# Performance work log

Hardware: AMD Instinct MI355X
Metric: run time of the kernel (lower is better)

## Reference

```python
import jax, jax.numpy as jnp
import numpy as np

B, T, DC, DS, H, V = 8, 1024, 128, 128, 512, 50000
LENGTHS = np.array([2, 4])  # dictionary word lengths for slot 0 and slot 1
LMAX = 4                    # ring-buffer size >= max word length


def setup_inputs() -> dict:
    key = jax.random.key(0)
    ks = jax.random.split(key, 12)
    s = 0.05
    return {
        "char_emb": jax.random.normal(ks[0], (B, T, DC), jnp.float32),
        "word_ids": jax.random.randint(ks[1], (B, T, 2), 0, V),
        "sense_table": jax.random.normal(ks[2], (V, DS), jnp.float32),
        "w_ih": jax.random.normal(ks[3], (DC, 3 * H), jnp.float32) * s,
        "w_hh": jax.random.normal(ks[4], (H, 3 * H), jnp.float32) * s,
        "b": jnp.zeros((3 * H,), jnp.float32),
        "aw_ih": jax.random.normal(ks[5], (DC, H), jnp.float32) * s,
        "aw_hh": jax.random.normal(ks[6], (H, H), jnp.float32) * s,
        "ab": jnp.zeros((H,), jnp.float32),
        "ww_ih": jax.random.normal(ks[7], (DS, 3 * H), jnp.float32) * s,
        "ww_hh": jax.random.normal(ks[8], (H, 3 * H), jnp.float32) * s,
        "wb": jnp.zeros((3 * H,), jnp.float32),
    }


def _forward(char_emb, word_ids, sense_table, w_ih, w_hh, b,
             aw_ih, aw_hh, ab, ww_ih, ww_hh, wb):
    H_ = w_hh.shape[0]
    T_ = char_emb.shape[1]
    lengths = jnp.asarray(LENGTHS)
    slot_idx = jnp.arange(2)

    def run_seq(x_seq, wid_seq):
        # pend: ring buffer of pending word-cell states [LMAX, 2, H]
        def step(carry, t):
            h, c, pend, pmask = carry
            x = x_seq[t]
            # --- MultiInputLSTMCell (char cell) ---
            gates = x @ w_ih + h @ w_hh + b              # [3H]
            i = jax.nn.sigmoid(gates[:H_])
            o = jax.nn.sigmoid(gates[H_:2 * H_])
            g = jnp.tanh(gates[2 * H_:])
            r = jnp.mod(t, LMAX)
            cins = pend[r]                                # [2, H] incoming word cells
            m = pmask[r].astype(x.dtype)                  # [2] validity
            alpha = jax.nn.sigmoid(x @ aw_ih + ab + cins @ aw_hh)  # [2, H]
            ea = jnp.exp(alpha) * m[:, None]
            ei = jnp.exp(i)
            denom = ei + ea.sum(0)
            c_lat = (ei * g + (ea * cins).sum(0)) / denom
            c_plain = (1.0 - i) * c + i * g               # c_num == 0 path: f = 1 - i
            c1 = jnp.where(pmask[r].any(), c_lat, c_plain)
            h1 = o * jnp.tanh(c1)
            # consume the ring slot for this timestep
            pend = pend.at[r].set(0.0)
            pmask = pmask.at[r].set(False)
            # --- WordLSTMCell for words starting at t ---
            xw = sense_table[wid_seq[t]]                  # [2, DS]
            wg = xw @ ww_ih + h1 @ ww_hh + wb             # [2, 3H]
            f = jax.nn.sigmoid(wg[:, :H_])
            iw = jax.nn.sigmoid(wg[:, H_:2 * H_])
            gw = jnp.tanh(wg[:, 2 * H_:])
            cw = f * c1 + iw * gw                         # [2, H]
            ends = t + lengths - 1
            valid = ends < T_
            wslots = jnp.mod(ends, LMAX)
            old = pend[wslots, slot_idx]
            pend = pend.at[wslots, slot_idx].set(jnp.where(valid[:, None], cw, old))
            pmask = pmask.at[wslots, slot_idx].set(valid | pmask[wslots, slot_idx])
            return (h1, c1, pend, pmask), (h1, c1)

        carry0 = (jnp.zeros((H_,), x_seq.dtype), jnp.zeros((H_,), x_seq.dtype),
                  jnp.zeros((LMAX, 2, H_), x_seq.dtype), jnp.zeros((LMAX, 2), bool))
        _, (hs, cs) = jax.lax.scan(step, carry0, jnp.arange(T_))
        return hs, cs

    hs, cs = jax.vmap(run_seq)(char_emb, word_ids)
    return jnp.stack((hs, cs))  # [2, B, T, H]


def reference(char_emb, word_ids, sense_table, w_ih, w_hh, b,
              aw_ih, aw_hh, ab, ww_ih, ww_hh, wb):
    return _forward(char_emb, word_ids, sense_table, w_ih, w_hh, b,
                    aw_ih, aw_hh, ab, ww_ih, ww_hh, wb)
```

## Files before the change

kernel.cpp:

```cpp
#include <hip/hip_runtime.h>
#include <hip/hip_bf16.h>


#define Bq 8
#define Tq 1024
#define DCq 128
#define Hq 512
#define NWG 32
#define NTHR 256

typedef unsigned long long u64;

#define HPUB_OFF  0u
#define PENDP_OFF 65536u
#define WIHT_OFF  327680u
#define WHHT_OFF  720896u
#define AWIHT_OFF 2293760u
#define AWHHT_OFF 2424832u
#define WWIHT_OFF 2949120u
#define WWHHT_OFF 3342336u

__device__ __forceinline__ float bflo(unsigned u){ return __uint_as_float(u << 16); }
__device__ __forceinline__ float bfhi(unsigned u){ return __uint_as_float(u & 0xffff0000u); }
__device__ __forceinline__ float sigm(float x){ return 1.0f / (1.0f + __expf(-x)); }

__device__ __forceinline__ unsigned f2bf(float f){
  unsigned u = __float_as_uint(f);
  u += 0x7fffu + ((u >> 16) & 1u);
  return u >> 16;
}

__device__ __forceinline__ void fma4(float& acc, uint2 w, float4 v){
  acc = fmaf(bflo(w.x), v.x, acc);
  acc = fmaf(bfhi(w.x), v.y, acc);
  acc = fmaf(bflo(w.y), v.z, acc);
  acc = fmaf(bfhi(w.y), v.w, acc);
}

__device__ __forceinline__ float red16(float x){
  x += __shfl_xor(x, 8, 16);
  x += __shfl_xor(x, 4, 16);
  x += __shfl_xor(x, 2, 16);
  x += __shfl_xor(x, 1, 16);
  return x;
}

__device__ __forceinline__ u64 pack64(float v, unsigned gen){
  return ((u64)gen << 32) | (u64)__float_as_uint(v);
}
__device__ __forceinline__ void st64(u64* p, u64 w){
  __hip_atomic_store(p, w, __ATOMIC_RELAXED, __HIP_MEMORY_SCOPE_AGENT);
}
__device__ __forceinline__ void pub64(u64* p, float v, unsigned gen){
  st64(p, pack64(v, gen));
}
__device__ __forceinline__ u64 ld64(const u64* p){
  return __hip_atomic_load(p, __ATOMIC_RELAXED, __HIP_MEMORY_SCOPE_AGENT);
}
__device__ __forceinline__ unsigned genof(u64 v){ return (unsigned)(v >> 32); }
__device__ __forceinline__ float valof(u64 v){ return __uint_as_float((unsigned)v); }

__global__ void transpose_bf16(const float* __restrict__ src, __hip_bfloat16* __restrict__ dst,
                               int kshift, int total, int N){
  const int K = 1 << kshift;
  for (int idx = blockIdx.x * blockDim.x + threadIdx.x; idx < total;
       idx += gridDim.x * blockDim.x){
    int n = idx >> kshift;
    int k = idx & (K - 1);
    dst[idx] = __float2bfloat16(src[(size_t)k * N + n]);
  }
}

__global__ void __launch_bounds__(NTHR, 1)
lattice_main(const float* __restrict__ char_emb,
             const int*   __restrict__ word_ids,
             const float* __restrict__ sense_table,
             const float* __restrict__ bias_b,
             const float* __restrict__ bias_ab,
             const float* __restrict__ bias_wb,
             unsigned char* __restrict__ ws,
             float* __restrict__ out)
{
  const int seq  = blockIdx.x;
  const int wg   = blockIdx.y;
  const int tid  = threadIdx.x;
  const int grp  = tid >> 4;
  const int lane = tid & 15;
  const int J    = wg * 16 + grp;
  const int i0   = tid * 2, i1 = tid * 2 + 1;

  u64* hpub = (u64*)(ws + HPUB_OFF)  + (size_t)seq * 2 * 256;
  u64* pnd  = (u64*)(ws + PENDP_OFF) + (size_t)seq * 4 * 2 * Hq;

  const uint2* w_ihT  = (const uint2*)(ws + WIHT_OFF);
  const uint2* w_hhT  = (const uint2*)(ws + WHHT_OFF);
  const uint2* aw_ihT = (const uint2*)(ws + AWIHT_OFF);
  const uint2* aw_hhT = (const uint2*)(ws + AWHHT_OFF);
  const uint2* ww_ihT = (const uint2*)(ws + WWIHT_OFF);
  const uint2* ww_hhT = (const uint2*)(ws + WWHHT_OFF);

  uint2 Rwhh_i[8], Rwhh_o[8], Rwhh_g[8], Rawhh[8];
  uint2 Rwwh_f[8], Rwwh_i[8], Rwwh_g[8];
  uint2 Rwih_i[2], Rwih_o[2], Rwih_g[2], Rawih[2];
  uint2 Rwwi_f[2], Rwwi_i[2], Rwwi_g[2];
  {
    const uint2* whh_i = w_hhT  + (size_t)(0*Hq + J) * 128;
    const uint2* whh_o = w_hhT  + (size_t)(1*Hq + J) * 128;
    const uint2* whh_g = w_hhT  + (size_t)(2*Hq + J) * 128;
    const uint2* awhh  = aw_hhT + (size_t)J * 128;
    const uint2* wwh_f = ww_hhT + (size_t)(0*Hq + J) * 128;
    const uint2* wwh_i = ww_hhT + (size_t)(1*Hq + J) * 128;
    const uint2* wwh_g = ww_hhT + (size_t)(2*Hq + J) * 128;
#pragma unroll
    for (int it = 0; it < 8; ++it){
      const int q = it * 16 + lane;
      Rwhh_i[it] = whh_i[q];  Rwhh_o[it] = whh_o[q];  Rwhh_g[it] = whh_g[q];
      Rawhh[it]  = awhh[q];
      Rwwh_f[it] = wwh_f[q];  Rwwh_i[it] = wwh_i[q];  Rwwh_g[it] = wwh_g[q];
    }
    const uint2* wih_i = w_ihT  + (size_t)(0*Hq + J) * 32;
    const uint2* wih_o = w_ihT  + (size_t)(1*Hq + J) * 32;
    const uint2* wih_g = w_ihT  + (size_t)(2*Hq + J) * 32;
    const uint2* awih  = aw_ihT + (size_t)J * 32;
    const uint2* wwi_f = ww_ihT + (size_t)(0*Hq + J) * 32;
    const uint2* wwi_i = ww_ihT + (size_t)(1*Hq + J) * 32;
    const uint2* wwi_g = ww_ihT + (size_t)(2*Hq + J) * 32;
#pragma unroll
    for (int it = 0; it < 2; ++it){
      const int q = it * 16 + lane;
      Rwih_i[it] = wih_i[q];  Rwih_o[it] = wih_o[q];  Rwih_g[it] = wih_g[q];
      Rawih[it]  = awih[q];
      Rwwi_f[it] = wwi_f[q];  Rwwi_i[it] = wwi_i[q];  Rwwi_g[it] = wwi_g[q];
    }
  }

  const float b_i  = bias_b[J], b_o = bias_b[Hq + J], b_g = bias_b[2*Hq + J];
  const float ab_J = bias_ab[J];
  const float wb_f = bias_wb[J], wb_i = bias_wb[Hq + J], wb_g = bias_wb[2*Hq + J];

  float* out_h = out + (size_t)seq * Tq * Hq;
  float* out_c = out + ((size_t)Bq + seq) * Tq * Hq;

  __shared__ __align__(16) float shH[2][Hq];
  __shared__ __align__(16) float sh_p0[Hq];
  __shared__ __align__(16) float sh_p1[Hq];
  __shared__ __align__(16) float shx[2][DCq];
  __shared__ __align__(16) float shxw0[2][DCq];
  __shared__ __align__(16) float shxw1[2][DCq];

  shH[0][i0] = 0.f; shH[0][i1] = 0.f;
  shH[1][i0] = 0.f; shH[1][i1] = 0.f;
  sh_p0[i0] = 0.f; sh_p0[i1] = 0.f;
  sh_p1[i0] = 0.f; sh_p1[i1] = 0.f;
  if (tid < DCq){
    shx[0][tid] = char_emb[((size_t)seq * Tq + 0) * DCq + tid];
  } else {
    const int k = tid - DCq;
    const int w0 = word_ids[(size_t)seq * Tq * 2 + 0];
    const int w1 = word_ids[(size_t)seq * Tq * 2 + 1];
    shxw0[0][k] = sense_table[(size_t)w0 * DCq + k];
    shxw1[0][k] = sense_table[(size_t)w1 * DCq + k];
  }
  __syncthreads();

  for (int t = 0; t < Tq; ++t){
    const int par = t & 1;
    const float* hprev = shH[par ^ 1];

    const u64* p0 = pnd + ((size_t)(t & 3) * 2 + 0) * Hq;
    const u64* p1 = pnd + ((size_t)(t & 3) * 2 + 1) * Hq;
    u64 qa = 0, qb = 0, qc = 0, qd = 0;
    if (t >= 1){ qa = ld64(p0 + i0); qb = ld64(p0 + i1); }
    if (t >= 3){ qc = ld64(p1 + i0); qd = ld64(p1 + i1); }

    float a_i = 0.f, a_o = 0.f, a_g = 0.f, a_xa = 0.f;
#pragma unroll
    for (int it = 0; it < 8; ++it){
      const int k0 = it * 64 + lane * 4;
      float4 hv = *(const float4*)(hprev + k0);
      fma4(a_i, Rwhh_i[it], hv);
      fma4(a_o, Rwhh_o[it], hv);
      fma4(a_g, Rwhh_g[it], hv);
    }
#pragma unroll
    for (int it = 0; it < 2; ++it){
      const int k0 = it * 64 + lane * 4;
      float4 xv = *(const float4*)(shx[par] + k0);
      fma4(a_i,  Rwih_i[it], xv);
      fma4(a_o,  Rwih_o[it], xv);
      fma4(a_g,  Rwih_g[it], xv);
      fma4(a_xa, Rawih[it],  xv);
    }
    a_i  = red16(a_i);  a_o  = red16(a_o);  a_g  = red16(a_g);  a_xa = red16(a_xa);

    if (t >= 3){
      const unsigned tg0 = (unsigned)t, tg1 = (unsigned)(t - 2);
      while (!(genof(qa) >= tg0 && genof(qb) >= tg0 &&
               genof(qc) >= tg1 && genof(qd) >= tg1)){
        qa = ld64(p0 + i0); qb = ld64(p0 + i1);
        qc = ld64(p1 + i0); qd = ld64(p1 + i1);
      }
      sh_p0[i0] = valof(qa); sh_p0[i1] = valof(qb);
      sh_p1[i0] = valof(qc); sh_p1[i1] = valof(qd);
    } else if (t >= 1){
      const unsigned tg0 = (unsigned)t;
      while (!(genof(qa) >= tg0 && genof(qb) >= tg0)){
        qa = ld64(p0 + i0); qb = ld64(p0 + i1);
      }
      sh_p0[i0] = valof(qa); sh_p0[i1] = valof(qb);
    }
    __syncthreads();

    float a_p0 = 0.f, a_p1 = 0.f;
#pragma unroll
    for (int it = 0; it < 8; ++it){
      const int k0 = it * 64 + lane * 4;
      float4 p0v = *(const float4*)(sh_p0 + k0);
      float4 p1v = *(const float4*)(sh_p1 + k0);
      fma4(a_p0, Rawhh[it], p0v);
      fma4(a_p1, Rawhh[it], p1v);
    }
    a_p0 = red16(a_p0); a_p1 = red16(a_p1);

    const float gi = sigm(a_i + b_i);
    const float go = sigm(a_o + b_o);
    const float gg = tanhf(a_g + b_g);
    float c1;
    if (t == 0){
      c1 = gi * gg;
    } else {
      const float base = a_xa + ab_J;
      const float ea0 = __expf(sigm(base + a_p0));
      const float ei  = __expf(gi);
      float num = ei * gg + ea0 * sh_p0[J];
      float den = ei + ea0;
      if (t >= 3){
        const float ea1 = __expf(sigm(base + a_p1));
        num += ea1 * sh_p1[J];
        den += ea1;
      }
      c1 = num / den;
    }
    const float h1 = go * tanhf(c1);
    const float h1o = __shfl_xor(h1, 16);
    if (lane == 0){
      if ((grp & 1) == 0){
        const u64 w = ((u64)(unsigned)(t + 1) << 32)
                    | ((u64)f2bf(h1o) << 16) | (u64)f2bf(h1);
        st64(hpub + (size_t)par * 256 + (J >> 1), w);
      }
      out_h[(size_t)t * Hq + J] = h1;
      out_c[(size_t)t * Hq + J] = c1;
    }

    float x_f0 = 0.f, x_i0 = 0.f, x_g0 = 0.f, x_f1 = 0.f, x_i1 = 0.f, x_g1 = 0.f;
#pragma unroll
    for (int it = 0; it < 2; ++it){
      const int k0 = it * 64 + lane * 4;
      float4 x0 = *(const float4*)(shxw0[par] + k0);
      float4 x1 = *(const float4*)(shxw1[par] + k0);
      fma4(x_f0, Rwwi_f[it], x0);  fma4(x_f1, Rwwi_f[it], x1);
      fma4(x_i0, Rwwi_i[it], x0);  fma4(x_i1, Rwwi_i[it], x1);
      fma4(x_g0, Rwwi_g[it], x0);  fma4(x_g1, Rwwi_g[it], x1);
    }
    x_f0 = red16(x_f0); x_i0 = red16(x_i0); x_g0 = red16(x_g0);
    x_f1 = red16(x_f1); x_i1 = red16(x_i1); x_g1 = red16(x_g1);
    {
      const int tn = (t + 1 < Tq) ? t + 1 : t;
      if (tid < DCq){
        shx[par ^ 1][tid] = char_emb[((size_t)seq * Tq + tn) * DCq + tid];
      } else {
        const int k = tid - DCq;
        const int w0 = word_ids[((size_t)seq * Tq + tn) * 2 + 0];
        const int w1 = word_ids[((size_t)seq * Tq + tn) * 2 + 1];
        shxw0[par ^ 1][k] = sense_table[(size_t)w0 * DCq + k];
        shxw1[par ^ 1][k] = sense_table[(size_t)w1 * DCq + k];
      }
    }

    {
      const u64* hp = hpub + (size_t)par * 256;
      const unsigned tg = (unsigned)(t + 1);
      u64 a = ld64(hp + tid);
      while (genof(a) < tg) a = ld64(hp + tid);
      shH[par][i0] = bflo((unsigned)a & 0xffffu);
      shH[par][i1] = bflo(((unsigned)a >> 16) & 0xffffu);
    }
    __syncthreads();

    float r_f = 0.f, r_i = 0.f, r_g = 0.f;
#pragma unroll
    for (int it = 0; it < 8; ++it){
      const int k0 = it * 64 + lane * 4;
      float4 hv = *(const float4*)(shH[par] + k0);
      fma4(r_f, Rwwh_f[it], hv);
      fma4(r_i, Rwwh_i[it], hv);
      fma4(r_g, Rwwh_g[it], hv);
    }
    r_f = red16(r_f); r_i = red16(r_i); r_g = red16(r_g);

    if (lane == 0){
      const float f0  = sigm(r_f + x_f0 + wb_f);
      const float iw0 = sigm(r_i + x_i0 + wb_i);
      const float g0  = tanhf(r_g + x_g0 + wb_g);
      const float cw0 = f0 * c1 + iw0 * g0;
      const float f1  = sigm(r_f + x_f1 + wb_f);
      const float iw1 = sigm(r_i + x_i1 + wb_i);
      const float g1  = tanhf(r_g + x_g1 + wb_g);
      const float cw1 = f1 * c1 + iw1 * g1;
      pub64(pnd + ((size_t)((t + 1) & 3) * 2 + 0) * Hq + J, cw0, (unsigned)(t + 1));
      pub64(pnd + ((size_t)((t + 3) & 3) * 2 + 1) * Hq + J, cw1, (unsigned)(t + 1));
    }
  }
}

extern "C" void kernel_launch(void* const* d_in, const int* in_sizes, int n_in,
                              void* d_out, int out_size, void* d_ws, size_t ws_size,
                              hipStream_t stream){
  const float* char_emb = (const float*)d_in[0];
  const int*   word_ids = (const int*)d_in[1];
  const float* sense    = (const float*)d_in[2];
  const float* w_ih     = (const float*)d_in[3];
  const float* w_hh     = (const float*)d_in[4];
  const float* bb       = (const float*)d_in[5];
  const float* aw_ih    = (const float*)d_in[6];
  const float* aw_hh    = (const float*)d_in[7];
  const float* ab       = (const float*)d_in[8];
  const float* ww_ih    = (const float*)d_in[9];
  const float* ww_hh    = (const float*)d_in[10];
  const float* wb       = (const float*)d_in[11];
  unsigned char* ws = (unsigned char*)d_ws;
  float* out = (float*)d_out;

  hipMemsetAsync(ws, 0, WIHT_OFF, stream);

  transpose_bf16<<<512, NTHR, 0, stream>>>(w_ih,  (__hip_bfloat16*)(ws + WIHT_OFF),  7, 128*1536, 1536);
  transpose_bf16<<<512, NTHR, 0, stream>>>(w_hh,  (__hip_bfloat16*)(ws + WHHT_OFF),  9, 512*1536, 1536);
  transpose_bf16<<<512, NTHR, 0, stream>>>(aw_ih, (__hip_bfloat16*)(ws + AWIHT_OFF), 7, 128*512,  512);
  transpose_bf16<<<512, NTHR, 0, stream>>>(aw_hh, (__hip_bfloat16*)(ws + AWHHT_OFF), 9, 512*512,  512);
  transpose_bf16<<<512, NTHR, 0, stream>>>(ww_ih, (__hip_bfloat16*)(ws + WWIHT_OFF), 7, 128*1536, 1536);
  transpose_bf16<<<512, NTHR, 0, stream>>>(ww_hh, (__hip_bfloat16*)(ws + WWHHT_OFF), 9, 512*1536, 1536);

  dim3 grid(Bq, NWG);
  lattice_main<<<grid, NTHR, 0, stream>>>(char_emb, word_ids, sense, bb, ab, wb, ws, out);
}
```

Measured before the change: 5.817 ms.

## Halve workgroups per sequence with 512-thread blocks and double-issued spin polls

Each sequence is now split over 16 workgroups of 512 threads (32 hidden units each) instead of 32 workgroups of 256, so fewer blocks take part in the per-step cross-workgroup handshake. Each thread now polls one pending entry, the spin loops keep two loads in flight, and the next-step input prefetch moves to the top of the step. Larger blocks raise per-CU register pressure, and the launch bound now allows two blocks per CU.

```diff
diff --git a/kernel.cpp b/kernel.cpp
--- a/kernel.cpp
+++ b/kernel.cpp
@@ -6,8 +6,9 @@
 #define Tq 1024
 #define DCq 128
 #define Hq 512
-#define NWG 32
-#define NTHR 256
+#define NWG 16
+#define NTHR 512
+#define NGRP 32
 
 typedef unsigned long long u64;
 
@@ -71,7 +72,7 @@
   }
 }
 
-__global__ void __launch_bounds__(NTHR, 1)
+__global__ void __launch_bounds__(NTHR, 2)
 lattice_main(const float* __restrict__ char_emb,
              const int*   __restrict__ word_ids,
              const float* __restrict__ sense_table,
@@ -86,8 +87,7 @@
   const int tid  = threadIdx.x;
   const int grp  = tid >> 4;
   const int lane = tid & 15;
-  const int J    = wg * 16 + grp;
-  const int i0   = tid * 2, i1 = tid * 2 + 1;
+  const int J    = wg * NGRP + grp;
 
   u64* hpub = (u64*)(ws + HPUB_OFF)  + (size_t)seq * 2 * 256;
   u64* pnd  = (u64*)(ws + PENDP_OFF) + (size_t)seq * 4 * 2 * Hq;
@@ -148,17 +148,19 @@
   __shared__ __align__(16) float shxw0[2][DCq];
   __shared__ __align__(16) float shxw1[2][DCq];
 
-  shH[0][i0] = 0.f; shH[0][i1] = 0.f;
-  shH[1][i0] = 0.f; shH[1][i1] = 0.f;
-  sh_p0[i0] = 0.f; sh_p0[i1] = 0.f;
-  sh_p1[i0] = 0.f; sh_p1[i1] = 0.f;
+  shH[0][tid & 511] = 0.f;
+  shH[1][tid & 511] = 0.f;
+  sh_p0[tid & 511] = 0.f;
+  sh_p1[tid & 511] = 0.f;
   if (tid < DCq){
     shx[0][tid] = char_emb[((size_t)seq * Tq + 0) * DCq + tid];
-  } else {
+  } else if (tid < 2 * DCq){
     const int k = tid - DCq;
     const int w0 = word_ids[(size_t)seq * Tq * 2 + 0];
+    shxw0[0][k] = sense_table[(size_t)w0 * DCq + k];
+  } else if (tid < 3 * DCq){
+    const int k = tid - 2 * DCq;
     const int w1 = word_ids[(size_t)seq * Tq * 2 + 1];
-    shxw0[0][k] = sense_table[(size_t)w0 * DCq + k];
     shxw1[0][k] = sense_table[(size_t)w1 * DCq + k];
   }
   __syncthreads();
@@ -167,11 +169,26 @@
     const int par = t & 1;
     const float* hprev = shH[par ^ 1];
 
-    const u64* p0 = pnd + ((size_t)(t & 3) * 2 + 0) * Hq;
-    const u64* p1 = pnd + ((size_t)(t & 3) * 2 + 1) * Hq;
-    u64 qa = 0, qb = 0, qc = 0, qd = 0;
-    if (t >= 1){ qa = ld64(p0 + i0); qb = ld64(p0 + i1); }
-    if (t >= 3){ qc = ld64(p1 + i0); qd = ld64(p1 + i1); }
+    {
+      const int tn = (t + 1 < Tq) ? t + 1 : t;
+      if (tid < DCq){
+        shx[par ^ 1][tid] = char_emb[((size_t)seq * Tq + tn) * DCq + tid];
+      } else if (tid < 2 * DCq){
+        const int k = tid - DCq;
+        const int w0 = word_ids[((size_t)seq * Tq + tn) * 2 + 0];
+        shxw0[par ^ 1][k] = sense_table[(size_t)w0 * DCq + k];
+      } else if (tid < 3 * DCq){
+        const int k = tid - 2 * DCq;
+        const int w1 = word_ids[((size_t)seq * Tq + tn) * 2 + 1];
+        shxw1[par ^ 1][k] = sense_table[(size_t)w1 * DCq + k];
+      }
+    }
+
+    const u64* p0 = pnd + ((size_t)(t & 3) * 2 + 0) * Hq + tid;
+    const u64* p1 = pnd + ((size_t)(t & 3) * 2 + 1) * Hq + tid;
+    u64 a0 = 0, a1 = 0;
+    if (t >= 1){ a0 = ld64(p0); }
+    if (t >= 3){ a1 = ld64(p1); }
 
     float a_i = 0.f, a_o = 0.f, a_g = 0.f, a_xa = 0.f;
 #pragma unroll
@@ -195,19 +212,25 @@
 
     if (t >= 3){
       const unsigned tg0 = (unsigned)t, tg1 = (unsigned)(t - 2);
-      while (!(genof(qa) >= tg0 && genof(qb) >= tg0 &&
-               genof(qc) >= tg1 && genof(qd) >= tg1)){
-        qa = ld64(p0 + i0); qb = ld64(p0 + i1);
-        qc = ld64(p1 + i0); qd = ld64(p1 + i1);
-      }
-      sh_p0[i0] = valof(qa); sh_p0[i1] = valof(qb);
-      sh_p1[i0] = valof(qc); sh_p1[i1] = valof(qd);
+      u64 b0 = ld64(p0), b1 = ld64(p1);
+      for (;;){
+        if (genof(a0) >= tg0 && genof(a1) >= tg1) break;
+        a0 = ld64(p0); a1 = ld64(p1);
+        if (genof(b0) >= tg0 && genof(b1) >= tg1){ a0 = b0; a1 = b1; break; }
+        b0 = ld64(p0); b1 = ld64(p1);
+      }
+      sh_p0[tid] = valof(a0);
+      sh_p1[tid] = valof(a1);
     } else if (t >= 1){
       const unsigned tg0 = (unsigned)t;
-      while (!(genof(qa) >= tg0 && genof(qb) >= tg0)){
-        qa = ld64(p0 + i0); qb = ld64(p0 + i1);
-      }
-      sh_p0[i0] = valof(qa); sh_p0[i1] = valof(qb);
+      u64 b0 = ld64(p0);
+      for (;;){
+        if (genof(a0) >= tg0) break;
+        a0 = ld64(p0);
+        if (genof(b0) >= tg0){ a0 = b0; break; }
+        b0 = ld64(p0);
+      }
+      sh_p0[tid] = valof(a0);
     }
     __syncthreads();
 
@@ -265,26 +288,19 @@
     }
     x_f0 = red16(x_f0); x_i0 = red16(x_i0); x_g0 = red16(x_g0);
     x_f1 = red16(x_f1); x_i1 = red16(x_i1); x_g1 = red16(x_g1);
-    {
-      const int tn = (t + 1 < Tq) ? t + 1 : t;
-      if (tid < DCq){
-        shx[par ^ 1][tid] = char_emb[((size_t)seq * Tq + tn) * DCq + tid];
-      } else {
-        const int k = tid - DCq;
-        const int w0 = word_ids[((size_t)seq * Tq + tn) * 2 + 0];
-        const int w1 = word_ids[((size_t)seq * Tq + tn) * 2 + 1];
-        shxw0[par ^ 1][k] = sense_table[(size_t)w0 * DCq + k];
-        shxw1[par ^ 1][k] = sense_table[(size_t)w1 * DCq + k];
-      }
-    }
-
-    {
-      const u64* hp = hpub + (size_t)par * 256;
+
+    if (tid < 256){
+      const u64* hp = hpub + (size_t)par * 256 + tid;
       const unsigned tg = (unsigned)(t + 1);
-      u64 a = ld64(hp + tid);
-      while (genof(a) < tg) a = ld64(hp + tid);
-      shH[par][i0] = bflo((unsigned)a & 0xffffu);
-      shH[par][i1] = bflo(((unsigned)a >> 16) & 0xffffu);
+      u64 a = ld64(hp), b = ld64(hp);
+      for (;;){
+        if (genof(a) >= tg) break;
+        a = ld64(hp);
+        if (genof(b) >= tg){ a = b; break; }
+        b = ld64(hp);
+      }
+      shH[par][2 * tid]     = bflo((unsigned)a & 0xffffu);
+      shH[par][2 * tid + 1] = bflo(((unsigned)a >> 16) & 0xffffu);
     }
     __syncthreads();
 
@@ -334,12 +350,12 @@
 
   hipMemsetAsync(ws, 0, WIHT_OFF, stream);
 
-  transpose_bf16<<<512, NTHR, 0, stream>>>(w_ih,  (__hip_bfloat16*)(ws + WIHT_OFF),  7, 128*1536, 1536);
-  transpose_bf16<<<512, NTHR, 0, stream>>>(w_hh,  (__hip_bfloat16*)(ws + WHHT_OFF),  9, 512*1536, 1536);
-  transpose_bf16<<<512, NTHR, 0, stream>>>(aw_ih, (__hip_bfloat16*)(ws + AWIHT_OFF), 7, 128*512,  512);
-  transpose_bf16<<<512, NTHR, 0, stream>>>(aw_hh, (__hip_bfloat16*)(ws + AWHHT_OFF), 9, 512*512,  512);
-  transpose_bf16<<<512, NTHR, 0, stream>>>(ww_ih, (__hip_bfloat16*)(ws + WWIHT_OFF), 7, 128*1536, 1536);
-  transpose_bf16<<<512, NTHR, 0, stream>>>(ww_hh, (__hip_bfloat16*)(ws + WWHHT_OFF), 9, 512*1536, 1536);
+  transpose_bf16<<<512, 256, 0, stream>>>(w_ih,  (__hip_bfloat16*)(ws + WIHT_OFF),  7, 128*1536, 1536);
+  transpose_bf16<<<512, 256, 0, stream>>>(w_hh,  (__hip_bfloat16*)(ws + WHHT_OFF),  9, 512*1536, 1536);
+  transpose_bf16<<<512, 256, 0, stream>>>(aw_ih, (__hip_bfloat16*)(ws + AWIHT_OFF), 7, 128*512,  512);
+  transpose_bf16<<<512, 256, 0, stream>>>(aw_hh, (__hip_bfloat16*)(ws + AWHHT_OFF), 9, 512*512,  512);
+  transpose_bf16<<<512, 256, 0, stream>>>(ww_ih, (__hip_bfloat16*)(ws + WWIHT_OFF), 7, 128*1536, 1536);
+  transpose_bf16<<<512, 256, 0, stream>>>(ww_hh, (__hip_bfloat16*)(ws + WWHHT_OFF), 9, 512*1536, 1536);
 
   dim3 grid(Bq, NWG);
   lattice_main<<<grid, NTHR, 0, stream>>>(char_emb, word_ids, sense, bb, ab, wb, ws, out);
```

Result: slower. 11.71 ms (+101.3%).

## Prefetch inputs into registers and overlap h-publish spin with word-input GEMV

Applied to the files above, without the earlier changes.

Next-step char embeddings and sense-table rows are now loaded directly into registers at the top of each step, replacing the double-buffered shared-memory staging. The hidden-state publish is moved earlier, and its first poll load is issued before the word-input dot products so the cross-workgroup wait overlaps that compute. The output stores of h and c are deferred until after the barrier, off the critical path. This costs more live registers, which may lower occupancy or cause spills, and changes the spin loop to double-issue loads.

```diff
diff --git a/kernel.cpp b/kernel.cpp
--- a/kernel.cpp
+++ b/kernel.cpp
@@ -144,28 +144,42 @@
   __shared__ __align__(16) float shH[2][Hq];
   __shared__ __align__(16) float sh_p0[Hq];
   __shared__ __align__(16) float sh_p1[Hq];
-  __shared__ __align__(16) float shx[2][DCq];
-  __shared__ __align__(16) float shxw0[2][DCq];
-  __shared__ __align__(16) float shxw1[2][DCq];
+
+  const int ka = lane * 4;
+  const int kb = 64 + lane * 4;
+  const float* cbase = char_emb + (size_t)seq * Tq * DCq;
+  const int*   wbase = word_ids + (size_t)seq * Tq * 2;
 
   shH[0][i0] = 0.f; shH[0][i1] = 0.f;
   shH[1][i0] = 0.f; shH[1][i1] = 0.f;
   sh_p0[i0] = 0.f; sh_p0[i1] = 0.f;
   sh_p1[i0] = 0.f; sh_p1[i1] = 0.f;
-  if (tid < DCq){
-    shx[0][tid] = char_emb[((size_t)seq * Tq + 0) * DCq + tid];
-  } else {
-    const int k = tid - DCq;
-    const int w0 = word_ids[(size_t)seq * Tq * 2 + 0];
-    const int w1 = word_ids[(size_t)seq * Tq * 2 + 1];
-    shxw0[0][k] = sense_table[(size_t)w0 * DCq + k];
-    shxw1[0][k] = sense_table[(size_t)w1 * DCq + k];
+  float4 xc0, xc1, xw0c0, xw0c1, xw1c0, xw1c1;
+  {
+    const int w0 = wbase[0], w1 = wbase[1];
+    xc0   = *(const float4*)(cbase + ka);
+    xc1   = *(const float4*)(cbase + kb);
+    xw0c0 = *(const float4*)(sense_table + (size_t)w0 * DCq + ka);
+    xw0c1 = *(const float4*)(sense_table + (size_t)w0 * DCq + kb);
+    xw1c0 = *(const float4*)(sense_table + (size_t)w1 * DCq + ka);
+    xw1c1 = *(const float4*)(sense_table + (size_t)w1 * DCq + kb);
   }
   __syncthreads();
+
+  float h1 = 0.f, c1 = 0.f;
 
   for (int t = 0; t < Tq; ++t){
     const int par = t & 1;
     const float* hprev = shH[par ^ 1];
+
+    const int tn = (t + 1 < Tq) ? t + 1 : t;
+    const int w0n = wbase[2 * tn], w1n = wbase[2 * tn + 1];
+    float4 xn0   = *(const float4*)(cbase + (size_t)tn * DCq + ka);
+    float4 xn1   = *(const float4*)(cbase + (size_t)tn * DCq + kb);
+    float4 xw0n0 = *(const float4*)(sense_table + (size_t)w0n * DCq + ka);
+    float4 xw0n1 = *(const float4*)(sense_table + (size_t)w0n * DCq + kb);
+    float4 xw1n0 = *(const float4*)(sense_table + (size_t)w1n * DCq + ka);
+    float4 xw1n1 = *(const float4*)(sense_table + (size_t)w1n * DCq + kb);
 
     const u64* p0 = pnd + ((size_t)(t & 3) * 2 + 0) * Hq;
     const u64* p1 = pnd + ((size_t)(t & 3) * 2 + 1) * Hq;
@@ -182,15 +196,10 @@
       fma4(a_o, Rwhh_o[it], hv);
       fma4(a_g, Rwhh_g[it], hv);
     }
-#pragma unroll
-    for (int it = 0; it < 2; ++it){
-      const int k0 = it * 64 + lane * 4;
-      float4 xv = *(const float4*)(shx[par] + k0);
-      fma4(a_i,  Rwih_i[it], xv);
-      fma4(a_o,  Rwih_o[it], xv);
-      fma4(a_g,  Rwih_g[it], xv);
-      fma4(a_xa, Rawih[it],  xv);
-    }
+    fma4(a_i,  Rwih_i[0], xc0);  fma4(a_i,  Rwih_i[1], xc1);
+    fma4(a_o,  Rwih_o[0], xc0);  fma4(a_o,  Rwih_o[1], xc1);
+    fma4(a_g,  Rwih_g[0], xc0);  fma4(a_g,  Rwih_g[1], xc1);
+    fma4(a_xa, Rawih[0],  xc0);  fma4(a_xa, Rawih[1],  xc1);
     a_i  = red16(a_i);  a_o  = red16(a_o);  a_g  = red16(a_g);  a_xa = red16(a_xa);
 
     if (t >= 3){
@@ -225,7 +234,6 @@
     const float gi = sigm(a_i + b_i);
     const float go = sigm(a_o + b_o);
     const float gg = tanhf(a_g + b_g);
-    float c1;
     if (t == 0){
       c1 = gi * gg;
     } else {
@@ -241,52 +249,44 @@
       }
       c1 = num / den;
     }
-    const float h1 = go * tanhf(c1);
+    h1 = go * tanhf(c1);
     const float h1o = __shfl_xor(h1, 16);
+    if (lane == 0 && (grp & 1) == 0){
+      const u64 w = ((u64)(unsigned)(t + 1) << 32)
+                  | ((u64)f2bf(h1o) << 16) | (u64)f2bf(h1);
+      st64(hpub + (size_t)par * 256 + (J >> 1), w);
+    }
+    const u64* hp = hpub + (size_t)par * 256 + tid;
+    u64 ha = ld64(hp);
+
+    float x_f0 = 0.f, x_i0 = 0.f, x_g0 = 0.f, x_f1 = 0.f, x_i1 = 0.f, x_g1 = 0.f;
+    fma4(x_f0, Rwwi_f[0], xw0c0);  fma4(x_f0, Rwwi_f[1], xw0c1);
+    fma4(x_i0, Rwwi_i[0], xw0c0);  fma4(x_i0, Rwwi_i[1], xw0c1);
+    fma4(x_g0, Rwwi_g[0], xw0c0);  fma4(x_g0, Rwwi_g[1], xw0c1);
+    fma4(x_f1, Rwwi_f[0], xw1c0);  fma4(x_f1, Rwwi_f[1], xw1c1);
+    fma4(x_i1, Rwwi_i[0], xw1c0);  fma4(x_i1, Rwwi_i[1], xw1c1);
+    fma4(x_g1, Rwwi_g[0], xw1c0);  fma4(x_g1, Rwwi_g[1], xw1c1);
+    x_f0 = red16(x_f0); x_i0 = red16(x_i0); x_g0 = red16(x_g0);
+    x_f1 = red16(x_f1); x_i1 = red16(x_i1); x_g1 = red16(x_g1);
+
+    {
+      const unsigned tg = (unsigned)(t + 1);
+      u64 b = ld64(hp);
+      for (;;){
+        if (genof(ha) >= tg) break;
+        ha = ld64(hp);
+        if (genof(b) >= tg){ ha = b; break; }
+        b = ld64(hp);
+      }
+      shH[par][i0] = bflo((unsigned)ha & 0xffffu);
+      shH[par][i1] = bflo(((unsigned)ha >> 16) & 0xffffu);
+    }
+    __syncthreads();
+
     if (lane == 0){
-      if ((grp & 1) == 0){
-        const u64 w = ((u64)(unsigned)(t + 1) << 32)
-                    | ((u64)f2bf(h1o) << 16) | (u64)f2bf(h1);
-        st64(hpub + (size_t)par * 256 + (J >> 1), w);
-      }
       out_h[(size_t)t * Hq + J] = h1;
       out_c[(size_t)t * Hq + J] = c1;
     }
-
-    float x_f0 = 0.f, x_i0 = 0.f, x_g0 = 0.f, x_f1 = 0.f, x_i1 = 0.f, x_g1 = 0.f;
-#pragma unroll
-    for (int it = 0; it < 2; ++it){
-      const int k0 = it * 64 + lane * 4;
-      float4 x0 = *(const float4*)(shxw0[par] + k0);
-      float4 x1 = *(const float4*)(shxw1[par] + k0);
-      fma4(x_f0, Rwwi_f[it], x0);  fma4(x_f1, Rwwi_f[it], x1);
-      fma4(x_i0, Rwwi_i[it], x0);  fma4(x_i1, Rwwi_i[it], x1);
-      fma4(x_g0, Rwwi_g[it], x0);  fma4(x_g1, Rwwi_g[it], x1);
-    }
-    x_f0 = red16(x_f0); x_i0 = red16(x_i0); x_g0 = red16(x_g0);
-    x_f1 = red16(x_f1); x_i1 = red16(x_i1); x_g1 = red16(x_g1);
-    {
-      const int tn = (t + 1 < Tq) ? t + 1 : t;
-      if (tid < DCq){
-        shx[par ^ 1][tid] = char_emb[((size_t)seq * Tq + tn) * DCq + tid];
-      } else {
-        const int k = tid - DCq;
-        const int w0 = word_ids[((size_t)seq * Tq + tn) * 2 + 0];
-        const int w1 = word_ids[((size_t)seq * Tq + tn) * 2 + 1];
-        shxw0[par ^ 1][k] = sense_table[(size_t)w0 * DCq + k];
-        shxw1[par ^ 1][k] = sense_table[(size_t)w1 * DCq + k];
-      }
-    }
-
-    {
-      const u64* hp = hpub + (size_t)par * 256;
-      const unsigned tg = (unsigned)(t + 1);
-      u64 a = ld64(hp + tid);
-      while (genof(a) < tg) a = ld64(hp + tid);
-      shH[par][i0] = bflo((unsigned)a & 0xffffu);
-      shH[par][i1] = bflo(((unsigned)a >> 16) & 0xffffu);
-    }
-    __syncthreads();
 
     float r_f = 0.f, r_i = 0.f, r_g = 0.f;
 #pragma unroll
@@ -311,6 +311,10 @@
       pub64(pnd + ((size_t)((t + 1) & 3) * 2 + 0) * Hq + J, cw0, (unsigned)(t + 1));
       pub64(pnd + ((size_t)((t + 3) & 3) * 2 + 1) * Hq + J, cw1, (unsigned)(t + 1));
     }
+
+    xc0 = xn0; xc1 = xn1;
+    xw0c0 = xw0n0; xw0c1 = xw0n1;
+    xw1c0 = xw1n0; xw1c1 = xw1n1;
   }
 }
 
@@ -334,12 +338,12 @@
 
   hipMemsetAsync(ws, 0, WIHT_OFF, stream);
 
-  transpose_bf16<<<512, NTHR, 0, stream>>>(w_ih,  (__hip_bfloat16*)(ws + WIHT_OFF),  7, 128*1536, 1536);
-  transpose_bf16<<<512, NTHR, 0, stream>>>(w_hh,  (__hip_bfloat16*)(ws + WHHT_OFF),  9, 512*1536, 1536);
-  transpose_bf16<<<512, NTHR, 0, stream>>>(aw_ih, (__hip_bfloat16*)(ws + AWIHT_OFF), 7, 128*512,  512);
-  transpose_bf16<<<512, NTHR, 0, stream>>>(aw_hh, (__hip_bfloat16*)(ws + AWHHT_OFF), 9, 512*512,  512);
-  transpose_bf16<<<512, NTHR, 0, stream>>>(ww_ih, (__hip_bfloat16*)(ws + WWIHT_OFF), 7, 128*1536, 1536);
-  transpose_bf16<<<512, NTHR, 0, stream>>>(ww_hh, (__hip_bfloat16*)(ws + WWHHT_OFF), 9, 512*1536, 1536);
+  transpose_bf16<<<512, 256, 0, stream>>>(w_ih,  (__hip_bfloat16*)(ws + WIHT_OFF),  7, 128*1536, 1536);
+  transpose_bf16<<<512, 256, 0, stream>>>(w_hh,  (__hip_bfloat16*)(ws + WHHT_OFF),  9, 512*1536, 1536);
+  transpose_bf16<<<512, 256, 0, stream>>>(aw_ih, (__hip_bfloat16*)(ws + AWIHT_OFF), 7, 128*512,  512);
+  transpose_bf16<<<512, 256, 0, stream>>>(aw_hh, (__hip_bfloat16*)(ws + AWHHT_OFF), 9, 512*512,  512);
+  transpose_bf16<<<512, 256, 0, stream>>>(ww_ih, (__hip_bfloat16*)(ws + WWIHT_OFF), 7, 128*1536, 1536);
+  transpose_bf16<<<512, 256, 0, stream>>>(ww_hh, (__hip_bfloat16*)(ws + WWHHT_OFF), 9, 512*1536, 1536);
 
   dim3 grid(Bq, NWG);
   lattice_main<<<grid, NTHR, 0, stream>>>(char_emb, word_ids, sense, bb, ab, wb, ws, out);
```

Result: slower. 5.950 ms (+2.3%).
